# Performance work log

Hardware: AMD Instinct MI355X
Metric: run time of the kernel (lower is better)

The kernel has to match this reference:

```python
import jax, jax.numpy as jnp
import numpy as np

jax.config.update("jax_enable_x64", True)

MEM = 33554432  # 2**25 bytes, stored as int64 (256 MB)
SHIFTS = jnp.arange(8, dtype=jnp.int64) * 8  # [0,8,...,56] little-endian byte shifts


def _read_int(memory, addr):
    # Read 8 bytes at addr (clamped, like torch) and assemble a little-endian int64.
    idx = jnp.clip(addr + jnp.arange(8, dtype=jnp.int64), 0, memory.shape[0] - 1)
    return jnp.sum(memory[idx] << SHIFTS)


def _masked_write_int(memory, addr, value, mask):
    # Scatter 8 bytes of `value` at addr (clamped), gated by scalar mask (0/1).
    idx = jnp.clip(addr + jnp.arange(8, dtype=jnp.int64), 0, memory.shape[0] - 1)
    new_bytes = (value >> SHIFTS) & 255
    return memory.at[idx].set(jnp.where(mask != 0, new_bytes, memory[idx]))


def _masked_write_byte(memory, addr, value, mask):
    idx = jnp.clip(addr, 0, memory.shape[0] - 1)
    return memory.at[idx].set(jnp.where(mask != 0, value & 255, memory[idx]))


def setup_inputs() -> dict:
    key = jax.random.key(0)
    memory = jax.random.randint(key, (MEM,), 0, 256, dtype=jnp.int64)
    return {
        "pc": jnp.int64(0),
        "sp": jnp.int64(MEM - 4096),
        "bp": jnp.int64(MEM - 4096),
        "ax": jnp.int64(7),
        "memory": memory,
    }


def reference(pc, sp, bp, ax, memory):
    pc = jnp.asarray(pc, jnp.int64); sp = jnp.asarray(sp, jnp.int64)
    bp = jnp.asarray(bp, jnp.int64); ax = jnp.asarray(ax, jnp.int64)
    zero = jnp.int64(0); one = jnp.int64(1)

    # fetch
    instruction = _read_int(memory, pc)
    opcode = instruction & 255
    imm = instruction >> 8  # arithmetic shift, matches torch

    stack_top = _read_int(memory, sp)
    mem_at_ax = _read_int(memory, ax)

    pc_plus_8 = pc + 8
    pc_eq_imm = imm
    ret_pc = _read_int(memory, bp + 8)

    sp_unchanged = sp; sp_minus_8 = sp - 8; sp_plus_8 = sp + 8; sp_plus_imm = sp + imm
    bp_unchanged = bp
    bp_from_stack = _read_int(memory, bp)

    # ALU outcomes (all computed branchlessly)
    ax_safe = jnp.where(ax == 0, one, ax)
    ax_eq_bp_plus_imm = bp + imm
    ax_eq_imm = imm
    ax_eq_mem_at_ax = mem_at_ax
    ax_eq_mem_byte = mem_at_ax & 255
    ax_add = stack_top + ax
    ax_sub = stack_top - ax
    ax_mul = stack_top * ax
    ax_div = stack_top // ax_safe
    ax_mod = stack_top % ax_safe
    ax_or = stack_top | ax
    ax_xor = stack_top ^ ax
    ax_and = stack_top & ax
    ax_shl = stack_top << (ax & 63)
    ax_shr = stack_top >> (ax & 63)
    ax_eq = (stack_top == ax).astype(jnp.int64)
    ax_ne = (stack_top != ax).astype(jnp.int64)
    ax_lt = (stack_top < ax).astype(jnp.int64)
    ax_gt = (stack_top > ax).astype(jnp.int64)
    ax_le = (stack_top <= ax).astype(jnp.int64)
    ax_ge = (stack_top >= ax).astype(jnp.int64)

    all_pc = jnp.stack([
        pc_plus_8, pc_plus_8, pc_eq_imm, pc_eq_imm,
        jnp.where(ax == 0, pc_eq_imm, pc_plus_8),
        jnp.where(ax != 0, pc_eq_imm, pc_plus_8),
        pc_plus_8, pc_plus_8, ret_pc,
        pc_plus_8, pc_plus_8, pc_plus_8, pc_plus_8, pc_plus_8, pc_plus_8,
        pc_plus_8, pc_plus_8, pc_plus_8, pc_plus_8, pc_plus_8, pc_plus_8,
        pc_plus_8, pc_plus_8, pc_plus_8, pc_plus_8, pc_plus_8, pc_plus_8,
        pc_plus_8, pc_plus_8, pc_plus_8, pc_plus_8, pc_plus_8, pc_plus_8,
        pc_plus_8, pc_plus_8, pc_plus_8, pc_plus_8, pc_plus_8, pc])
    all_sp = jnp.stack([
        sp_unchanged, sp_unchanged, sp_unchanged, sp_minus_8, sp_unchanged,
        sp_unchanged, sp - 8 - imm, sp_plus_imm, bp + 16, sp_unchanged,
        sp_unchanged, sp_plus_8, sp_plus_8, sp_minus_8, sp_plus_8, sp_plus_8,
        sp_plus_8, sp_plus_8, sp_plus_8, sp_plus_8, sp_plus_8, sp_plus_8,
        sp_plus_8, sp_plus_8, sp_plus_8, sp_plus_8, sp_plus_8, sp_plus_8,
        sp_plus_8, sp_plus_8, sp_unchanged, sp_unchanged, sp_unchanged,
        sp_unchanged, sp_unchanged, sp_unchanged, sp_unchanged, sp_unchanged,
        sp_unchanged])
    all_bp = jnp.stack(
        [bp_unchanged] * 6 + [sp - 8, bp_unchanged, bp_from_stack] + [bp_unchanged] * 30)
    all_ax = jnp.stack([
        ax_eq_bp_plus_imm, ax_eq_imm, ax, ax, ax, ax, ax, ax, ax,
        ax_eq_mem_at_ax, ax_eq_mem_byte, ax, ax, ax,
        ax_add, ax_sub, ax_mul, ax_div, ax_mod, ax_or, ax_xor, ax_and,
        ax_shl, ax_shr, ax_eq, ax_ne, ax_lt, ax_gt, ax_le, ax_ge,
        zero, zero, zero, zero, zero, zero, zero, zero, ax])

    opcode_idx = jnp.clip(opcode, 0, 38)
    new_pc = all_pc[opcode_idx]
    new_sp = all_sp[opcode_idx]
    new_bp = all_bp[opcode_idx]
    new_ax = all_ax[opcode_idx]

    # masked memory writes (PSH/JSR/ENT push; SI/SC store)
    is_psh = (opcode == 13).astype(jnp.int64)
    is_jsr = (opcode == 3).astype(jnp.int64)
    is_ent = (opcode == 6).astype(jnp.int64)
    is_si = (opcode == 11).astype(jnp.int64)
    is_sc = (opcode == 12).astype(jnp.int64)
    push_addr = sp - 8
    push_value = is_psh * ax + is_jsr * (pc + 8) + is_ent * bp
    needs_push = is_psh + is_jsr + is_ent

    new_memory = _masked_write_int(memory, push_addr, push_value, needs_push)
    new_memory = _masked_write_int(new_memory, stack_top, ax, is_si)
    new_memory = _masked_write_byte(new_memory, stack_top, ax & 255, is_sc)

    halted = opcode == 38
    return (new_pc, new_sp, new_bp, new_ax, new_memory, halted)
```

## Files before the change

### kernel.cpp

```cpp
#include <hip/hip_runtime.h>


static constexpr long long MEMN = 33554432LL;
static constexpr int NT = 256;
static constexpr int NB = 4096;
static constexpr int ITERS = 8;

typedef int   v4i __attribute__((ext_vector_type(4)));
typedef float v4f __attribute__((ext_vector_type(4)));

__device__ __forceinline__ long long clamp_idx(long long a) {
    return a < 0 ? 0 : (a > MEMN - 1 ? MEMN - 1 : a);
}

__device__ __forceinline__ long long rd_byte(const void* mem, int flag, long long idx) {
    long long j = clamp_idx(idx);
    if (flag == 2) return (long long)((const float*)mem)[j];
    if (flag == 1) return (long long)((const int*)mem)[j << 1];
    return (long long)((const int*)mem)[j];
}

__device__ __forceinline__ long long rd_int(const void* mem, int flag, long long addr) {
    unsigned long long v = 0;
    #pragma unroll
    for (int k = 0; k < 8; ++k)
        v |= (unsigned long long)(unsigned int)rd_byte(mem, flag, addr + k) << (8 * k);
    return (long long)v;
}

__device__ __forceinline__ long long rd_scalar(const void* p, int flag) {
    if (flag == 2) return (long long)((const float*)p)[0];
    return (long long)((const int*)p)[0];
}

__device__ __forceinline__ v4i patch4(v4i f, long long i, int nw, int lo, int hi,
                                      const int* s_idx, const int* s_val) {
    if (nw) {
        int base = (int)(i << 2);
        if (base + 3 >= lo && base <= hi) {
            #pragma unroll
            for (int e = 0; e < 4; ++e)
                for (int t = 0; t < nw; ++t)
                    if (s_idx[t] == base + e) f[e] = s_val[t];
        }
    }
    return f;
}

__global__ __launch_bounds__(NT) void fused_step(const void* pc_b, const void* sp_b,
                                                 const void* bp_b, const void* ax_b,
                                                 const void* mem_b, int* out) {
    __shared__ int s_flag, s_nw, s_lo, s_hi;
    __shared__ int s_idx[8], s_val[8];

    const int* mi = (const int*)mem_b;

    if (threadIdx.x < 64) {
        unsigned int w = (unsigned int)mi[threadIdx.x];
        unsigned long long big    = __ballot(w > 255u);
        unsigned long long oddnz  = __ballot(((threadIdx.x & 1) != 0) && (w != 0u));
        if (threadIdx.x == 0) {
            int flag = big ? 2 : (oddnz ? 0 : 1);
            s_flag = flag;

            long long pc = rd_scalar(pc_b, flag);
            long long sp = rd_scalar(sp_b, flag);
            long long bp = rd_scalar(bp_b, flag);
            long long ax = rd_scalar(ax_b, flag);

            long long ins       = rd_int(mem_b, flag, pc);
            long long opcode    = ins & 255;
            long long imm       = ins >> 8;
            long long stack_top = rd_int(mem_b, flag, sp);
            long long mem_at_ax = rd_int(mem_b, flag, ax);
            long long ret_pc    = rd_int(mem_b, flag, bp + 8);
            long long bp_stack  = rd_int(mem_b, flag, bp);
            long long pc8       = (long long)((unsigned long long)pc + 8ULL);

            unsigned long long ust = (unsigned long long)stack_top;
            unsigned long long uax = (unsigned long long)ax;
            long long ax_safe = (ax == 0) ? 1LL : ax;
            long long q, r;
            if (ax_safe == -1LL) { q = (long long)(0ULL - ust); r = 0; }
            else {
                q = stack_top / ax_safe; r = stack_top % ax_safe;
                if (r != 0 && ((r < 0) != (ax_safe < 0))) { q -= 1; r += ax_safe; }
            }
            int sh = (int)(ax & 63);

            long long op = opcode > 38 ? 38 : opcode;
            long long npc = pc8, nsp = sp, nbp = bp, nax = ax;
            switch ((int)op) {
                case 0:  nax = (long long)((unsigned long long)bp + (unsigned long long)imm); break;
                case 1:  nax = imm; break;
                case 2:  npc = imm; break;
                case 3:  npc = imm; nsp = sp - 8; break;
                case 4:  npc = (ax == 0) ? imm : pc8; break;
                case 5:  npc = (ax != 0) ? imm : pc8; break;
                case 6:  nsp = sp - 8 - imm; nbp = sp - 8; break;
                case 7:  nsp = sp + imm; break;
                case 8:  npc = ret_pc; nsp = bp + 16; nbp = bp_stack; break;
                case 9:  nax = mem_at_ax; break;
                case 10: nax = mem_at_ax & 255; break;
                case 11: nsp = sp + 8; break;
                case 12: nsp = sp + 8; break;
                case 13: nsp = sp - 8; break;
                case 14: nsp = sp + 8; nax = (long long)(ust + uax); break;
                case 15: nsp = sp + 8; nax = (long long)(ust - uax); break;
                case 16: nsp = sp + 8; nax = (long long)(ust * uax); break;
                case 17: nsp = sp + 8; nax = q; break;
                case 18: nsp = sp + 8; nax = r; break;
                case 19: nsp = sp + 8; nax = stack_top | ax; break;
                case 20: nsp = sp + 8; nax = stack_top ^ ax; break;
                case 21: nsp = sp + 8; nax = stack_top & ax; break;
                case 22: nsp = sp + 8; nax = (long long)(ust << sh); break;
                case 23: nsp = sp + 8; nax = stack_top >> sh; break;
                case 24: nsp = sp + 8; nax = (stack_top == ax) ? 1 : 0; break;
                case 25: nsp = sp + 8; nax = (stack_top != ax) ? 1 : 0; break;
                case 26: nsp = sp + 8; nax = (stack_top <  ax) ? 1 : 0; break;
                case 27: nsp = sp + 8; nax = (stack_top >  ax) ? 1 : 0; break;
                case 28: nsp = sp + 8; nax = (stack_top <= ax) ? 1 : 0; break;
                case 29: nsp = sp + 8; nax = (stack_top >= ax) ? 1 : 0; break;
                case 38: npc = pc; break;
                default: nax = 0; break;
            }

            int nw = 0, lo = 0x7fffffff, hi = -1;
            long long waddr = 0; unsigned long long wval = 0; int wbytes = 0;
            if (opcode == 13 || opcode == 3 || opcode == 6) {
                waddr = sp - 8;
                wval = (unsigned long long)(opcode == 13 ? ax : (opcode == 3 ? pc8 : bp));
                wbytes = 8;
            } else if (opcode == 11) {
                waddr = stack_top; wval = (unsigned long long)ax; wbytes = 8;
            } else if (opcode == 12) {
                waddr = stack_top; wval = (unsigned long long)(ax & 255); wbytes = 1;
            }
            for (int k = 0; k < wbytes; ++k) {
                int j = (int)clamp_idx(waddr + k);
                s_idx[nw] = j;
                s_val[nw] = (int)((wval >> (8 * k)) & 255ULL);
                lo = j < lo ? j : lo;
                hi = j > hi ? j : hi;
                ++nw;
            }
            s_nw = nw; s_lo = lo; s_hi = hi;

            if (blockIdx.x == 0) {
                out[0] = (int)npc;
                out[1] = (int)nsp;
                out[2] = (int)nbp;
                out[3] = (int)nax;
                out[4 + MEMN] = (opcode == 38) ? 1 : 0;
            }
        }
    }
    __syncthreads();

    const int  flag = s_flag;
    const int  nw   = s_nw;
    const int  lo   = s_lo;
    const int  hi   = s_hi;
    v4i* o = (v4i*)(out + 4);

    if (flag == 1) {
        const v4i* m = (const v4i*)mem_b;
        const int lane = threadIdx.x & 63;
        const long long gw = (long long)((blockIdx.x * NT + threadIdx.x) >> 6);
        const long long NW = (long long)NB * NT / 64;
        const int slX = (2 * lane) & 63;
        const int slY = (2 * lane + 1) & 63;
        const bool loA = lane < 32;
        #pragma unroll
        for (int k = 0; k < ITERS; ++k) {
            const long long W = (gw + (long long)k * NW) << 6;
            v4i A = m[2 * W + lane];
            v4i B = m[2 * W + 64 + lane];
            int a0 = __shfl(A[0], slX, 64), b0 = __shfl(B[0], slX, 64);
            int a2 = __shfl(A[2], slX, 64), b2 = __shfl(B[2], slX, 64);
            int c0 = __shfl(A[0], slY, 64), d0 = __shfl(B[0], slY, 64);
            int c2 = __shfl(A[2], slY, 64), d2 = __shfl(B[2], slY, 64);
            v4i f;
            f[0] = loA ? a0 : b0;
            f[1] = loA ? a2 : b2;
            f[2] = loA ? c0 : d0;
            f[3] = loA ? c2 : d2;
            const long long i = W + lane;
            f = patch4(f, i, nw, lo, hi, s_idx, s_val);
            o[i] = f;
        }
    } else if (flag == 0) {
        const v4i* m = (const v4i*)mem_b;
        const long long tid = (long long)blockIdx.x * NT + threadIdx.x;
        const long long TOT = (long long)NB * NT;
        #pragma unroll
        for (int k = 0; k < ITERS; ++k) {
            long long i = tid + (long long)k * TOT;
            v4i f = m[i];
            f = patch4(f, i, nw, lo, hi, s_idx, s_val);
            o[i] = f;
        }
    } else {
        const v4f* m = (const v4f*)mem_b;
        const long long tid = (long long)blockIdx.x * NT + threadIdx.x;
        const long long TOT = (long long)NB * NT;
        #pragma unroll
        for (int k = 0; k < ITERS; ++k) {
            long long i = tid + (long long)k * TOT;
            v4f a = m[i];
            v4i f; f[0] = (int)a[0]; f[1] = (int)a[1]; f[2] = (int)a[2]; f[3] = (int)a[3];
            f = patch4(f, i, nw, lo, hi, s_idx, s_val);
            o[i] = f;
        }
    }
}

extern "C" void kernel_launch(void* const* d_in, const int* in_sizes, int n_in,
                              void* d_out, int out_size, void* d_ws, size_t ws_size,
                              hipStream_t stream) {
    int* out = (int*)d_out;
    fused_step<<<NB, NT, 0, stream>>>(d_in[0], d_in[1], d_in[2], d_in[3], d_in[4], out);
}
```

Measured before the change: 252.3 us.

## Replace unrolled shuffle-based copy with grid-stride loop and halve block count

The fixed 8-iteration unrolled copy with wave shuffles, used for the int64 input layout, becomes a simple grid-stride loop. Each thread now loads two adjacent 16-byte vectors and picks the low words directly. The grid drops from 4096 to 2048 blocks, so each thread handles more elements in a runtime loop. This removes the shuffle instructions and rebalances work per thread, at the cost of strided-by-two per-thread loads and less unrolling.

```diff
diff --git a/kernel.cpp b/kernel.cpp
--- a/kernel.cpp
+++ b/kernel.cpp
@@ -3,8 +3,7 @@
 
 static constexpr long long MEMN = 33554432LL;
 static constexpr int NT = 256;
-static constexpr int NB = 4096;
-static constexpr int ITERS = 8;
+static constexpr int NB = 2048;
 
 typedef int   v4i __attribute__((ext_vector_type(4)));
 typedef float v4f __attribute__((ext_vector_type(4)));
@@ -161,52 +160,29 @@
     const int  nw   = s_nw;
     const int  lo   = s_lo;
     const int  hi   = s_hi;
+    const long long tid    = (long long)blockIdx.x * NT + threadIdx.x;
+    const long long stride = (long long)NB * NT;
+    const long long nvec   = MEMN / 4;
     v4i* o = (v4i*)(out + 4);
 
     if (flag == 1) {
         const v4i* m = (const v4i*)mem_b;
-        const int lane = threadIdx.x & 63;
-        const long long gw = (long long)((blockIdx.x * NT + threadIdx.x) >> 6);
-        const long long NW = (long long)NB * NT / 64;
-        const int slX = (2 * lane) & 63;
-        const int slY = (2 * lane + 1) & 63;
-        const bool loA = lane < 32;
-        #pragma unroll
-        for (int k = 0; k < ITERS; ++k) {
-            const long long W = (gw + (long long)k * NW) << 6;
-            v4i A = m[2 * W + lane];
-            v4i B = m[2 * W + 64 + lane];
-            int a0 = __shfl(A[0], slX, 64), b0 = __shfl(B[0], slX, 64);
-            int a2 = __shfl(A[2], slX, 64), b2 = __shfl(B[2], slX, 64);
-            int c0 = __shfl(A[0], slY, 64), d0 = __shfl(B[0], slY, 64);
-            int c2 = __shfl(A[2], slY, 64), d2 = __shfl(B[2], slY, 64);
-            v4i f;
-            f[0] = loA ? a0 : b0;
-            f[1] = loA ? a2 : b2;
-            f[2] = loA ? c0 : d0;
-            f[3] = loA ? c2 : d2;
-            const long long i = W + lane;
+        for (long long i = tid; i < nvec; i += stride) {
+            v4i a = m[2 * i];
+            v4i b = m[2 * i + 1];
+            v4i f; f[0] = a[0]; f[1] = a[2]; f[2] = b[0]; f[3] = b[2];
             f = patch4(f, i, nw, lo, hi, s_idx, s_val);
             o[i] = f;
         }
     } else if (flag == 0) {
         const v4i* m = (const v4i*)mem_b;
-        const long long tid = (long long)blockIdx.x * NT + threadIdx.x;
-        const long long TOT = (long long)NB * NT;
-        #pragma unroll
-        for (int k = 0; k < ITERS; ++k) {
-            long long i = tid + (long long)k * TOT;
-            v4i f = m[i];
-            f = patch4(f, i, nw, lo, hi, s_idx, s_val);
+        for (long long i = tid; i < nvec; i += stride) {
+            v4i f = patch4(m[i], i, nw, lo, hi, s_idx, s_val);
             o[i] = f;
         }
     } else {
         const v4f* m = (const v4f*)mem_b;
-        const long long tid = (long long)blockIdx.x * NT + threadIdx.x;
-        const long long TOT = (long long)NB * NT;
-        #pragma unroll
-        for (int k = 0; k < ITERS; ++k) {
-            long long i = tid + (long long)k * TOT;
+        for (long long i = tid; i < nvec; i += stride) {
             v4f a = m[i];
             v4i f; f[0] = (int)a[0]; f[1] = (int)a[1]; f[2] = (int)a[2]; f[3] = (int)a[3];
             f = patch4(f, i, nw, lo, hi, s_idx, s_val);
```

Measured after the change: 250.3 us. No clear change (-0.8%).
